# Performance work log

Measured on AMD Instinct MI355X. Metric: run time of the kernel, lower is better.

The kernel has to match this reference:

```python
import jax, jax.numpy as jnp
import numpy as np

EPS = 1e-5

def _mlp(x, W1, b1, W2, b2):
    h = jax.nn.gelu(x @ W1 + b1, approximate=False)
    return h @ W2 + b2

def _ln(x, g, b):
    m = jnp.mean(x, axis=-1, keepdims=True)
    v = jnp.mean((x - m) ** 2, axis=-1, keepdims=True)
    return (x - m) * jax.lax.rsqrt(v + EPS) * g + b

def setup_inputs() -> dict:
    key = jax.random.key(0)
    B, N, D = 4, 256, 128
    ks = jax.random.split(key, 32)
    s = 0.02
    inp = {
        "node_h": jax.random.normal(ks[0], (B, N, D), jnp.float32),
        "pair_h": jax.random.normal(ks[1], (B, N, N, D), jnp.float32),
        "node_mask": jax.random.randint(ks[2], (B, N), 0, 2, jnp.int32),
        "edge_mask": jax.random.randint(ks[3], (B, N, N), 0, 2, jnp.int32),
        # node_from_pair MLP: 3D -> 2D -> D
        "nfp_W1": jax.random.normal(ks[4], (3 * D, 2 * D), jnp.float32) * s,
        "nfp_b1": jnp.zeros((2 * D,), jnp.float32),
        "nfp_W2": jax.random.normal(ks[5], (2 * D, D), jnp.float32) * s,
        "nfp_b2": jnp.zeros((D,), jnp.float32),
        # pair_from_node MLP: 5D -> 2D -> D
        "pfn_W1": jax.random.normal(ks[6], (5 * D, 2 * D), jnp.float32) * s,
        "pfn_b1": jnp.zeros((2 * D,), jnp.float32),
        "pfn_W2": jax.random.normal(ks[7], (2 * D, D), jnp.float32) * s,
        "pfn_b2": jnp.zeros((D,), jnp.float32),
        # node_ff: D -> 4D -> D
        "nff_W1": jax.random.normal(ks[8], (D, 4 * D), jnp.float32) * s,
        "nff_b1": jnp.zeros((4 * D,), jnp.float32),
        "nff_W2": jax.random.normal(ks[9], (4 * D, D), jnp.float32) * s,
        "nff_b2": jnp.zeros((D,), jnp.float32),
        # pair_ff: D -> 4D -> D
        "pff_W1": jax.random.normal(ks[10], (D, 4 * D), jnp.float32) * s,
        "pff_b1": jnp.zeros((4 * D,), jnp.float32),
        "pff_W2": jax.random.normal(ks[11], (4 * D, D), jnp.float32) * s,
        "pff_b2": jnp.zeros((D,), jnp.float32),
        # gates: 2D -> D, sigmoid
        "og_W": jax.random.normal(ks[12], (2 * D, D), jnp.float32) * s,
        "og_b": jnp.zeros((D,), jnp.float32),
        "ig_W": jax.random.normal(ks[13], (2 * D, D), jnp.float32) * s,
        "ig_b": jnp.zeros((D,), jnp.float32),
        # LayerNorms
        "nn1_g": jnp.ones((D,), jnp.float32), "nn1_b": jnp.zeros((D,), jnp.float32),
        "nn2_g": jnp.ones((D,), jnp.float32), "nn2_b": jnp.zeros((D,), jnp.float32),
        "pn1_g": jnp.ones((D,), jnp.float32), "pn1_b": jnp.zeros((D,), jnp.float32),
        "pn2_g": jnp.ones((D,), jnp.float32), "pn2_b": jnp.zeros((D,), jnp.float32),
    }
    return inp

def reference(node_h, pair_h, node_mask, edge_mask,
              nfp_W1, nfp_b1, nfp_W2, nfp_b2,
              pfn_W1, pfn_b1, pfn_W2, pfn_b2,
              nff_W1, nff_b1, nff_W2, nff_b2,
              pff_W1, pff_b1, pff_W2, pff_b2,
              og_W, og_b, ig_W, ig_b,
              nn1_g, nn1_b, nn2_g, nn2_b,
              pn1_g, pn1_b, pn2_g, pn2_b):
    vp = edge_mask.astype(jnp.float32)                       # [B,N,N]
    pair_m = pair_h * vp[..., None]                          # masked pairs
    out_deg = jnp.clip(vp.sum(axis=2), 1.0)[..., None]       # [B,N,1]
    in_deg = jnp.clip(vp.sum(axis=1), 1.0)[..., None]        # [B,N,1]
    out_ctx_raw = pair_m.sum(axis=2) / out_deg               # [B,N,D]
    in_ctx_raw = pair_m.sum(axis=1) / in_deg                 # [B,N,D]
    out_g = jax.nn.sigmoid(jnp.concatenate([node_h, out_ctx_raw], -1) @ og_W + og_b)
    in_g = jax.nn.sigmoid(jnp.concatenate([node_h, in_ctx_raw], -1) @ ig_W + ig_b)
    node_upd = _mlp(jnp.concatenate([node_h, out_g * out_ctx_raw, in_g * in_ctx_raw], -1),
                    nfp_W1, nfp_b1, nfp_W2, nfp_b2)
    node_h = _ln(node_h + node_upd, nn1_g, nn1_b)
    node_h = _ln(node_h + _mlp(node_h, nff_W1, nff_b1, nff_W2, nff_b2), nn2_g, nn2_b)
    node_h = node_h * node_mask.astype(jnp.float32)[..., None]

    B, N, D = node_h.shape
    hi = jnp.broadcast_to(node_h[:, :, None, :], (B, N, N, D))
    hj = jnp.broadcast_to(node_h[:, None, :, :], (B, N, N, D))
    feat = jnp.concatenate([pair_h, hi, hj, hi - hj, hi * hj], -1)  # [B,N,N,5D]
    pair_upd = _mlp(feat, pfn_W1, pfn_b1, pfn_W2, pfn_b2)
    pair_h = _ln(pair_h + pair_upd, pn1_g, pn1_b)
    pair_h = _ln(pair_h + _mlp(pair_h, pff_W1, pff_b1, pff_W2, pff_b2), pn2_g, pn2_b)
    pair_h = pair_h * vp[..., None]
    return (node_h, pair_h)
```

## Files before the change

### kernel.cpp

```cpp
#include <hip/hip_runtime.h>
#include <hip/hip_bf16.h>

#define DI __device__ __forceinline__

typedef float f32x4 __attribute__((ext_vector_type(4)));
typedef float f32x2 __attribute__((ext_vector_type(2)));
typedef short s16x8 __attribute__((ext_vector_type(8)));
typedef short s16x4 __attribute__((ext_vector_type(4)));
typedef unsigned u32x2 __attribute__((ext_vector_type(2)));
typedef unsigned u32x4 __attribute__((ext_vector_type(4)));

DI short f2bf(float x) {
  union { float f; unsigned u; } v; v.f = x;
  unsigned r = v.u + 0x7fffu + ((v.u >> 16) & 1u);
  return (short)(r >> 16);
}

DI float bf2f(short x) {
  union { unsigned u; float f; } v;
  v.u = ((unsigned)(unsigned short)x) << 16;
  return v.f;
}

DI unsigned cvt_pk(float lo, float hi) {
  unsigned r;
  asm("v_cvt_pk_bf16_f32 %0, %1, %2" : "=v"(r) : "v"(lo), "v"(hi));
  return r;
}

DI s16x8 pack8(f32x4 a, f32x4 b) {
  union { u32x4 u; s16x8 s; } r;
  r.u[0] = cvt_pk(a[0], a[1]); r.u[1] = cvt_pk(a[2], a[3]);
  r.u[2] = cvt_pk(b[0], b[1]); r.u[3] = cvt_pk(b[2], b[3]);
  return r.s;
}

DI float gelu_f(float x) {
  const float e = __expf(-x * fmaf(x * x, 0.0713548162f, 1.5957691216f));
  return __fdividef(x, 1.f + e);
}

__global__ __launch_bounds__(256) void prep_ctx_kernel(
    const float* __restrict__ pair_h, const int* __restrict__ edge_mask,
    const float* __restrict__ pfnW1, const float* __restrict__ pfnW2,
    const float* __restrict__ pffW1, const float* __restrict__ pffW2,
    short* __restrict__ W1b, float* __restrict__ Wu, short* __restrict__ W2T,
    short* __restrict__ W1Tp, short* __restrict__ W2Tp,
    float* __restrict__ out_ctx, float* __restrict__ in_ctx) {
  __shared__ float sacc[2][128];
  __shared__ float sdeg[2];
  const int t = threadIdx.x;
  if (blockIdx.x >= 2048) {
    int idx = (blockIdx.x - 2048) * 256 + t;
    if (idx < 98304) {
      int n = idx / 384, k = idx % 384;
      float v;
      if (k < 128) v = pfnW1[k * 256 + n];
      else if (k < 256) v = pfnW1[(128 + k) * 256 + n] - pfnW1[(256 + k) * 256 + n];
      else v = pfnW1[(256 + k) * 256 + n];
      W1b[idx] = f2bf(v);
      return;
    }
    idx -= 98304;
    if (idx < 32768) {
      int k = idx / 256, n = idx % 256;
      Wu[idx] = pfnW1[(128 + k) * 256 + n] + pfnW1[(384 + k) * 256 + n];
      return;
    }
    idx -= 32768;
    if (idx < 32768) {
      int n = idx / 256, k = idx % 256;
      W2T[idx] = f2bf(pfnW2[k * 128 + n]);
      return;
    }
    idx -= 32768;
    if (idx < 65536) {
      int n = idx / 128, k = idx % 128;
      W1Tp[idx] = f2bf(pffW1[k * 512 + n]);
      return;
    }
    idx -= 65536;
    if (idx < 65536) {
      int n = idx / 512, k = idx % 512;
      W2Tp[idx] = f2bf(pffW2[k * 128 + n]);
    }
    return;
  }
  const int wg = blockIdx.x;
  const int half = t >> 7, d = t & 127;
  const bool outmode = wg < 1024;
  const int w2 = outmode ? wg : wg - 1024;
  const int b = w2 >> 8, x = w2 & 255;
  float acc = 0.f, deg = 0.f;
  for (int y0 = 0; y0 < 256; y0 += 2) {
    const int y = y0 + half;
    int row;
    if (outmode) row = (b * 256 + x) * 256 + y;
    else row = (b * 256 + y) * 256 + x;
    const int m = edge_mask[row];
    if (m) {
      acc += pair_h[(long)row * 128 + d];
      deg += 1.f;
    }
  }
  sacc[half][d] = acc;
  if (d == 0) sdeg[half] = deg;
  __syncthreads();
  if (t < 128) {
    float tot = sacc[0][d] + sacc[1][d];
    float dg = fmaxf(sdeg[0] + sdeg[1], 1.f);
    float* dst = outmode ? out_ctx : in_ctx;
    dst[(b * 256 + x) * 128 + d] = tot / dg;
  }
}

__global__ __launch_bounds__(256) void node_kernel(
    const float* __restrict__ node_h, const float* __restrict__ out_ctx,
    const float* __restrict__ in_ctx, const int* __restrict__ node_mask,
    const float* __restrict__ ogW, const float* __restrict__ ogb,
    const float* __restrict__ igW, const float* __restrict__ igb,
    const float* __restrict__ nW1, const float* __restrict__ nb1,
    const float* __restrict__ nW2, const float* __restrict__ nb2,
    const float* __restrict__ fW1, const float* __restrict__ fb1,
    const float* __restrict__ fW2, const float* __restrict__ fb2,
    const float* __restrict__ g1, const float* __restrict__ be1,
    const float* __restrict__ g2, const float* __restrict__ be2,
    const float* __restrict__ Wu, const float* __restrict__ ub1,
    float* __restrict__ out_node, short* __restrict__ node_bf,
    float* __restrict__ u_all) {
  __shared__ float sh[4][1792];
  __shared__ float fin[8][128];
  const int t = threadIdx.x;
  const int wv = t >> 6, lane = t & 63;
  float* const xn = sh[wv];
  float* const xo = sh[wv] + 256;
  float* const xi = sh[wv] + 512;
  float* const hh = sh[wv] + 768;
  const int row0 = blockIdx.x * 8 + wv * 2;

#pragma unroll
  for (int r = 0; r < 2; ++r) {
    const int row = row0 + r;
#pragma unroll
    for (int c = 0; c < 2; ++c) {
      const int col = lane + 64 * c;
      xn[r * 128 + col] = node_h[row * 128 + col];
      xo[r * 128 + col] = out_ctx[row * 128 + col];
      xi[r * 128 + col] = in_ctx[row * 128 + col];
    }
  }
  __syncthreads();

  {
    float ao[2][2], ai[2][2];
#pragma unroll
    for (int c = 0; c < 2; ++c) {
      const int col = lane + 64 * c;
      ao[0][c] = ao[1][c] = ogb[col];
      ai[0][c] = ai[1][c] = igb[col];
    }
    for (int k = 0; k < 256; ++k) {
      float xo0, xo1, xi0, xi1;
      if (k < 128) {
        xo0 = xi0 = xn[k];
        xo1 = xi1 = xn[128 + k];
      } else {
        xo0 = xo[k - 128]; xo1 = xo[k];
        xi0 = xi[k - 128]; xi1 = xi[k];
      }
#pragma unroll
      for (int c = 0; c < 2; ++c) {
        const int col = lane + 64 * c;
        const float wo = ogW[k * 128 + col], wi = igW[k * 128 + col];
        ao[0][c] += xo0 * wo; ao[1][c] += xo1 * wo;
        ai[0][c] += xi0 * wi; ai[1][c] += xi1 * wi;
      }
    }
#pragma unroll
    for (int c = 0; c < 2; ++c) {
      const int col = lane + 64 * c;
#pragma unroll
      for (int r = 0; r < 2; ++r) {
// ... 84 lines not shown
      }
    }
#pragma unroll
    for (int c = 0; c < 8; ++c) {
      const int col = lane + 64 * c;
      hh[col] = gelu_f(af[0][c]);
      hh[512 + col] = gelu_f(af[1][c]);
    }
  }
  __syncthreads();
  {
    float a2[2][2];
#pragma unroll
    for (int c = 0; c < 2; ++c) {
      const int col = lane + 64 * c;
      a2[0][c] = a2[1][c] = fb2[col];
    }
    for (int k = 0; k < 512; ++k) {
      const float h0 = hh[k], h1 = hh[512 + k];
#pragma unroll
      for (int c = 0; c < 2; ++c) {
        const int col = lane + 64 * c;
        const float w = fW2[k * 128 + col];
        a2[0][c] += h0 * w; a2[1][c] += h1 * w;
      }
    }
#pragma unroll
    for (int r = 0; r < 2; ++r) {
      const int row = row0 + r;
      float v0 = xn[r * 128 + lane] + a2[r][0];
      float v1 = xn[r * 128 + lane + 64] + a2[r][1];
      float s = v0 + v1, ss = v0 * v0 + v1 * v1;
#pragma unroll
      for (int off = 1; off < 64; off <<= 1) {
        s += __shfl_xor(s, off, 64);
        ss += __shfl_xor(ss, off, 64);
      }
      const float m = s * (1.f / 128.f);
      const float var = ss * (1.f / 128.f) - m * m;
      const float rs = rsqrtf(var + 1e-5f);
      const float msk = (float)node_mask[row];
      const float o0 = ((v0 - m) * rs * g2[lane] + be2[lane]) * msk;
      const float o1 = ((v1 - m) * rs * g2[lane + 64] + be2[lane + 64]) * msk;
      out_node[row * 128 + lane] = o0;
      out_node[row * 128 + lane + 64] = o1;
      node_bf[row * 128 + lane] = f2bf(o0);
      node_bf[row * 128 + lane + 64] = f2bf(o1);
      fin[wv * 2 + r][lane] = o0;
      fin[wv * 2 + r][lane + 64] = o1;
    }
  }
  __syncthreads();
  {
    float uacc[8];
    const float bb = ub1[t];
#pragma unroll
    for (int r = 0; r < 8; ++r) uacc[r] = bb;
#pragma unroll 4
    for (int k = 0; k < 128; ++k) {
      const float w = Wu[k * 256 + t];
#pragma unroll
      for (int r = 0; r < 8; ++r) uacc[r] += fin[r][k] * w;
    }
#pragma unroll
    for (int r = 0; r < 8; ++r)
      u_all[(blockIdx.x * 8 + r) * 256 + t] = uacc[r];
  }
}

__global__ __launch_bounds__(512, 4) void pair_kernel(
    const float* __restrict__ pair_h, const short* __restrict__ node_bf,
    const int* __restrict__ edge_mask, const short* __restrict__ W1b,
    const short* __restrict__ W2T, const short* __restrict__ W1Tp,
    const short* __restrict__ W2Tp, const float* __restrict__ u_all,
    const float* __restrict__ b2, const float* __restrict__ b1p,
    const float* __restrict__ b2p, const float* __restrict__ g1,
    const float* __restrict__ be1, const float* __restrict__ g2,
    const float* __restrict__ be2, float* __restrict__ out_pair) {
  constexpr int OFF_A = 0, OFF_H1 = 0, OFF_Y = 0, OFF_H2 = 16384,
                OFF_SCR = 49152;
  __shared__ __align__(16) char smem[51200];

  const int t = threadIdx.x;
  const int wg = blockIdx.x;
  const int b = wg >> 10, rem = wg & 1023;
  const int i = rem >> 2, j0 = (rem & 3) << 6;
  const int bi = (b << 8) + i;
  const long rowbase = (long)bi * 256 + j0;

  const int lane = t & 63, wv = t >> 6;
  const int lr = lane & 15, lq = lane >> 4;
  const int swz = (lr & 7) << 4;
  const int jb = (wv >> 2) * 32, nb2 = (wv & 3) * 32;

  {
    const int r = t >> 3, oc = t & 7, c0 = oc * 16;
    const int rsw = (r & 7) << 4;
    const float* prow = pair_h + (rowbase + r) * 128 + c0;
    const short* hjrow = node_bf + (b * 256 + j0 + r) * 128 + c0;
    const short* hirow = node_bf + (b * 256 + i) * 128 + c0;
    char* arow = smem + OFF_A + r * 768;
#pragma unroll
    for (int h = 0; h < 2; ++h) {
      f32x4 p0 = *(const f32x4*)(prow + h * 8);
      f32x4 p1 = *(const f32x4*)(prow + h * 8 + 4);
      s16x8 hj = *(const s16x8*)(hjrow + h * 8);
      s16x8 hi = *(const s16x8*)(hirow + h * 8);
      *(s16x8*)(arow + ((c0 * 2 + h * 16) ^ rsw)) = pack8(p0, p1);
      *(s16x8*)(arow + ((256 + c0 * 2 + h * 16) ^ rsw)) = hj;
      union { u32x4 u; s16x8 s; } pd;
#pragma unroll
      for (int e = 0; e < 4; ++e)
        pd.u[e] = cvt_pk(bf2f(hi[2 * e]) * bf2f(hj[2 * e]),
                         bf2f(hi[2 * e + 1]) * bf2f(hj[2 * e + 1]));
      *(s16x8*)(arow + ((512 + c0 * 2 + h * 16) ^ rsw)) = pd.s;
    }
  }
  __syncthreads();

  f32x4 acc1[4][2];
#pragma unroll
  for (int jt = 0; jt < 4; ++jt)
#pragma unroll
    for (int nt = 0; nt < 2; ++nt) acc1[jt][nt] = {0.f, 0.f, 0.f, 0.f};
  {
    const int nb = wv * 32;
    const short* wp0 = W1b + (nb + lr) * 384 + lq * 8;
    const short* wp1 = W1b + (nb + 16 + lr) * 384 + lq * 8;
    s16x8 w0p[4], w1p[4];
#pragma unroll
    for (int pf = 0; pf < 4; ++pf) {
      w0p[pf] = *(const s16x8*)(wp0 + pf * 32);
      w1p[pf] = *(const s16x8*)(wp1 + pf * 32);
    }
    s16x8 dc[4];
#pragma unroll
    for (int jt = 0; jt < 4; ++jt)
      dc[jt] = *(const s16x8*)(smem + OFF_A +
                               (((jt * 16 + lr) * 768 + lq * 16) ^ swz));
#pragma unroll
    for (int ks = 0; ks < 12; ++ks) {
      s16x8 w0 = w0p[ks & 3], w1 = w1p[ks & 3];
      if (ks < 8) {
        w0p[ks & 3] = *(const s16x8*)(wp0 + (ks + 4) * 32);
        w1p[ks & 3] = *(const s16x8*)(wp1 + (ks + 4) * 32);
      }
      s16x8 d[4];
#pragma unroll
      for (int jt = 0; jt < 4; ++jt) d[jt] = dc[jt];
      if (ks < 11) {
#pragma unroll
        for (int jt = 0; jt < 4; ++jt)
          dc[jt] = *(const s16x8*)(smem + OFF_A +
                                   (((jt * 16 + lr) * 768 + (ks + 1) * 64 + lq * 16) ^ swz));
      }
#pragma unroll
      for (int jt = 0; jt < 4; ++jt) {
        acc1[jt][0] = __builtin_amdgcn_mfma_f32_16x16x32_bf16(w0, d[jt], acc1[jt][0], 0, 0, 0);
        acc1[jt][1] = __builtin_amdgcn_mfma_f32_16x16x32_bf16(w1, d[jt], acc1[jt][1], 0, 0, 0);
      }
    }
  }
  f32x4 bu0 = *(const f32x4*)(u_all + bi * 256 + wv * 32 + lq * 4);
  f32x4 bu1 = *(const f32x4*)(u_all + bi * 256 + wv * 32 + 16 + lq * 4);
  const short* q2p0 = W2T + (nb2 + lr) * 256 + lq * 8;
  const short* q2p1 = W2T + (nb2 + 16 + lr) * 256 + lq * 8;
  s16x8 q2w0[4], q2w1[4];
  q2w0[0] = *(const s16x8*)q2p0;
  q2w1[0] = *(const s16x8*)q2p1;
  q2w0[1] = *(const s16x8*)(q2p0 + 32);
  q2w1[1] = *(const s16x8*)(q2p1 + 32);
  __syncthreads();
  {
    const int nb = wv * 32;
#pragma unroll
    for (int nt = 0; nt < 2; ++nt) {
      const int n0 = nb + nt * 16 + lq * 4;
      const f32x4 bu = nt ? bu1 : bu0;
#pragma unroll
      for (int jt = 0; jt < 4; ++jt) {
        const int j = jt * 16 + lr;
        u32x2 pk = {cvt_pk(gelu_f(acc1[jt][nt][0] + bu[0]),
                           gelu_f(acc1[jt][nt][1] + bu[1])),
                    cvt_pk(gelu_f(acc1[jt][nt][2] + bu[2]),
                           gelu_f(acc1[jt][nt][3] + bu[3]))};
        *(u32x2*)(smem + OFF_H1 + ((j * 512 + n0 * 2) ^ swz)) = pk;
      }
    }
  }
  __syncthreads();

  f32x4 x1v[2][2];
  {
    q2w0[2] = *(const s16x8*)(q2p0 + 64);
    q2w1[2] = *(const s16x8*)(q2p1 + 64);
    q2w0[3] = *(const s16x8*)(q2p0 + 96);
    q2w1[3] = *(const s16x8*)(q2p1 + 96);
    f32x4 pr[2][2];
#pragma unroll
    for (int nt = 0; nt < 2; ++nt)
#pragma unroll
      for (int jt = 0; jt < 2; ++jt)
        pr[jt][nt] = *(const f32x4*)(pair_h + (rowbase + jb + jt * 16 + lr) * 128 +
                                     nb2 + nt * 16 + lq * 4);
    s16x8 dc[2];
#pragma unroll
    for (int jt = 0; jt < 2; ++jt)
      dc[jt] = *(const s16x8*)(smem + OFF_H1 +
                               (((jb + jt * 16 + lr) * 512 + lq * 16) ^ swz));
    f32x4 acc2[2][2];
#pragma unroll
    for (int jt = 0; jt < 2; ++jt)
#pragma unroll
      for (int nt = 0; nt < 2; ++nt) acc2[jt][nt] = {0.f, 0.f, 0.f, 0.f};
#pragma unroll
    for (int ks = 0; ks < 8; ++ks) {
      s16x8 w0 = q2w0[ks & 3], w1 = q2w1[ks & 3];
      if (ks < 4) {
        q2w0[ks & 3] = *(const s16x8*)(q2p0 + (ks + 4) * 32);
        q2w1[ks & 3] = *(const s16x8*)(q2p1 + (ks + 4) * 32);
      }
      s16x8 d[2];
#pragma unroll
      for (int jt = 0; jt < 2; ++jt) d[jt] = dc[jt];
      if (ks < 7) {
#pragma unroll
        for (int jt = 0; jt < 2; ++jt)
          dc[jt] = *(const s16x8*)(smem + OFF_H1 +
                                   (((jb + jt * 16 + lr) * 512 + (ks + 1) * 64 + lq * 16) ^ swz));
      }
#pragma unroll
      for (int jt = 0; jt < 2; ++jt) {
        acc2[jt][0] = __builtin_amdgcn_mfma_f32_16x16x32_bf16(w0, d[jt], acc2[jt][0], 0, 0, 0);
        acc2[jt][1] = __builtin_amdgcn_mfma_f32_16x16x32_bf16(w1, d[jt], acc2[jt][1], 0, 0, 0);
      }
    }
#pragma unroll
    for (int nt = 0; nt < 2; ++nt) {
      const int n0 = nb2 + nt * 16 + lq * 4;
      f32x4 bv = *(const f32x4*)(b2 + n0);
#pragma unroll
      for (int jt = 0; jt < 2; ++jt)
        x1v[jt][nt] = acc2[jt][nt] + bv + pr[jt][nt];
    }
  }
  {
    float s[2], ss[2];
#pragma unroll
    for (int jt = 0; jt < 2; ++jt) {
      s[jt] = 0.f; ss[jt] = 0.f;
#pragma unroll
      for (int nt = 0; nt < 2; ++nt)
#pragma unroll
        for (int v = 0; v < 4; ++v) {
          const float x = x1v[jt][nt][v];
          s[jt] += x; ss[jt] += x * x;
        }
      s[jt] += __shfl_xor(s[jt], 16, 64);
      ss[jt] += __shfl_xor(ss[jt], 16, 64);
      s[jt] += __shfl_xor(s[jt], 32, 64);
      ss[jt] += __shfl_xor(ss[jt], 32, 64);
    }
    if (lq == 0) {
#pragma unroll
      for (int jt = 0; jt < 2; ++jt) {
        const int j = jb + jt * 16 + lr;
        f32x2 p = {s[jt], ss[jt]};
        *(f32x2*)(smem + OFF_SCR + j * 32 + (wv & 3) * 8) = p;
      }
    }
    __syncthreads();
    float lnm[2], lnr[2];
#pragma unroll
    for (int jt = 0; jt < 2; ++jt) {
      const int j = jb + jt * 16 + lr;
      f32x4 pA = *(const f32x4*)(smem + OFF_SCR + j * 32);
      f32x4 pB = *(const f32x4*)(smem + OFF_SCR + j * 32 + 16);
      const float S = pA[0] + pA[2] + pB[0] + pB[2];
      const float SS = pA[1] + pA[3] + pB[1] + pB[3];
      const float m = S * (1.f / 128.f);
      const float var = SS * (1.f / 128.f) - m * m;
      lnm[jt] = m;
      lnr[jt] = rsqrtf(var + 1e-5f);
    }
#pragma unroll
    for (int nt = 0; nt < 2; ++nt) {
      const int n0 = nb2 + nt * 16 + lq * 4;
      f32x4 gv = *(const f32x4*)(g1 + n0);
      f32x4 bv = *(const f32x4*)(be1 + n0);
#pragma unroll
      for (int jt = 0; jt < 2; ++jt) {
        const int j = jb + jt * 16 + lr;
        float y[4];
#pragma unroll
        for (int v = 0; v < 4; ++v)
          y[v] = (x1v[jt][nt][v] - lnm[jt]) * lnr[jt] * gv[v] + bv[v];
        u32x2 pk = {cvt_pk(y[0], y[1]), cvt_pk(y[2], y[3])};
        *(u32x2*)(smem + OFF_Y + ((j * 256 + n0 * 2) ^ swz)) = pk;
      }
    }
  }
  const short* g3p0a = W1Tp + (wv * 32 + lr) * 128 + lq * 8;
  const short* g3p1a = W1Tp + (wv * 32 + 16 + lr) * 128 + lq * 8;
  s16x8 g3w0[4], g3w1[4];
  g3w0[0] = *(const s16x8*)g3p0a;
  g3w1[0] = *(const s16x8*)g3p1a;
  g3w0[1] = *(const s16x8*)(g3p0a + 32);
  g3w1[1] = *(const s16x8*)(g3p1a + 32);
  const int em0 = edge_mask[rowbase + jb + lr];
  const int em1 = edge_mask[rowbase + jb + 16 + lr];
  __syncthreads();

  f32x4 acc4[2][2];
#pragma unroll
  for (int jt = 0; jt < 2; ++jt)
#pragma unroll
    for (int nt = 0; nt < 2; ++nt) acc4[jt][nt] = {0.f, 0.f, 0.f, 0.f};

#pragma unroll
  for (int p = 0; p < 2; ++p) {
    f32x4 acc3[4][2];
#pragma unroll
    for (int jt = 0; jt < 4; ++jt)
#pragma unroll
      for (int nt = 0; nt < 2; ++nt) acc3[jt][nt] = {0.f, 0.f, 0.f, 0.f};
    {
      const int nb3 = p * 256 + wv * 32;
      const short* wp0 = W1Tp + (nb3 + lr) * 128 + lq * 8;
      const short* wp1 = W1Tp + (nb3 + 16 + lr) * 128 + lq * 8;
      if (p == 0) {
        g3w0[2] = *(const s16x8*)(wp0 + 64);
        g3w1[2] = *(const s16x8*)(wp1 + 64);
        g3w0[3] = *(const s16x8*)(wp0 + 96);
        g3w1[3] = *(const s16x8*)(wp1 + 96);
      } else {
#pragma unroll
        for (int pf = 0; pf < 4; ++pf) {
          g3w0[pf] = *(const s16x8*)(wp0 + pf * 32);
          g3w1[pf] = *(const s16x8*)(wp1 + pf * 32);
        }
      }
#pragma unroll
      for (int ks = 0; ks < 4; ++ks) {
        s16x8 d[4];
#pragma unroll
        for (int jt = 0; jt < 4; ++jt)
          d[jt] = *(const s16x8*)(smem + OFF_Y +
                                  (((jt * 16 + lr) * 256 + ks * 64 + lq * 16) ^ swz));
#pragma unroll
        for (int jt = 0; jt < 4; ++jt) {
          acc3[jt][0] = __builtin_amdgcn_mfma_f32_16x16x32_bf16(g3w0[ks], d[jt], acc3[jt][0], 0, 0, 0);
          acc3[jt][1] = __builtin_amdgcn_mfma_f32_16x16x32_bf16(g3w1[ks], d[jt], acc3[jt][1], 0, 0, 0);
        }
      }
    }
    const short* qp0 = W2Tp + (nb2 + lr) * 512 + p * 256 + lq * 8;
    const short* qp1 = W2Tp + (nb2 + 16 + lr) * 512 + p * 256 + lq * 8;
    s16x8 q4w0[4], q4w1[4];
    q4w0[0] = *(const s16x8*)qp0;
    q4w1[0] = *(const s16x8*)qp1;
    q4w0[1] = *(const s16x8*)(qp0 + 32);
    q4w1[1] = *(const s16x8*)(qp1 + 32);
    if (p == 1) __syncthreads();
    {
#pragma unroll
      for (int nt = 0; nt < 2; ++nt) {
        const int n0l = wv * 32 + nt * 16 + lq * 4;
        f32x4 bv = *(const f32x4*)(b1p + p * 256 + n0l);
#pragma unroll
        for (int jt = 0; jt < 4; ++jt) {
          const int j = jt * 16 + lr;
          u32x2 pk = {cvt_pk(gelu_f(acc3[jt][nt][0] + bv[0]),
                             gelu_f(acc3[jt][nt][1] + bv[1])),
                      cvt_pk(gelu_f(acc3[jt][nt][2] + bv[2]),
                             gelu_f(acc3[jt][nt][3] + bv[3]))};
          *(u32x2*)(smem + OFF_H2 + ((j * 512 + n0l * 2) ^ swz)) = pk;
        }
      }
    }
    __syncthreads();
    {
      q4w0[2] = *(const s16x8*)(qp0 + 64);
      q4w1[2] = *(const s16x8*)(qp1 + 64);
      q4w0[3] = *(const s16x8*)(qp0 + 96);
      q4w1[3] = *(const s16x8*)(qp1 + 96);
      s16x8 dc[2];
#pragma unroll
      for (int jt = 0; jt < 2; ++jt)
        dc[jt] = *(const s16x8*)(smem + OFF_H2 +
                                 (((jb + jt * 16 + lr) * 512 + lq * 16) ^ swz));
#pragma unroll
      for (int ks = 0; ks < 8; ++ks) {
        s16x8 w0 = q4w0[ks & 3], w1 = q4w1[ks & 3];
        if (ks < 4) {
          q4w0[ks & 3] = *(const s16x8*)(qp0 + (ks + 4) * 32);
          q4w1[ks & 3] = *(const s16x8*)(qp1 + (ks + 4) * 32);
        }
        s16x8 d[2];
#pragma unroll
        for (int jt = 0; jt < 2; ++jt) d[jt] = dc[jt];
        if (ks < 7) {
#pragma unroll
          for (int jt = 0; jt < 2; ++jt)
            dc[jt] = *(const s16x8*)(smem + OFF_H2 +
                                     (((jb + jt * 16 + lr) * 512 + (ks + 1) * 64 + lq * 16) ^ swz));
        }
#pragma unroll
        for (int jt = 0; jt < 2; ++jt) {
          acc4[jt][0] = __builtin_amdgcn_mfma_f32_16x16x32_bf16(w0, d[jt], acc4[jt][0], 0, 0, 0);
          acc4[jt][1] = __builtin_amdgcn_mfma_f32_16x16x32_bf16(w1, d[jt], acc4[jt][1], 0, 0, 0);
        }
      }
    }
  }

  f32x4 x2v[2][2];
#pragma unroll
  for (int nt = 0; nt < 2; ++nt) {
    const int n0 = nb2 + nt * 16 + lq * 4;
    f32x4 bv = *(const f32x4*)(b2p + n0);
#pragma unroll
    for (int jt = 0; jt < 2; ++jt) {
      const int j = jb + jt * 16 + lr;
      s16x4 yv = *(const s16x4*)(smem + OFF_Y + ((j * 256 + n0 * 2) ^ swz));
      f32x4 yr;
#pragma unroll
      for (int v = 0; v < 4; ++v) yr[v] = bf2f(yv[v]);
      x2v[jt][nt] = acc4[jt][nt] + bv + yr;
    }
  }
  {
    float s[2], ss[2];
#pragma unroll
    for (int jt = 0; jt < 2; ++jt) {
      s[jt] = 0.f; ss[jt] = 0.f;
#pragma unroll
      for (int nt = 0; nt < 2; ++nt)
#pragma unroll
        for (int v = 0; v < 4; ++v) {
          const float x = x2v[jt][nt][v];
          s[jt] += x; ss[jt] += x * x;
        }
      s[jt] += __shfl_xor(s[jt], 16, 64);
      ss[jt] += __shfl_xor(ss[jt], 16, 64);
      s[jt] += __shfl_xor(s[jt], 32, 64);
      ss[jt] += __shfl_xor(ss[jt], 32, 64);
    }
    if (lq == 0) {
#pragma unroll
      for (int jt = 0; jt < 2; ++jt) {
        const int j = jb + jt * 16 + lr;
        f32x2 p = {s[jt], ss[jt]};
        *(f32x2*)(smem + OFF_SCR + j * 32 + (wv & 3) * 8) = p;
      }
    }
    __syncthreads();
    float lnm[2], lnr[2], vp[2];
#pragma unroll
    for (int jt = 0; jt < 2; ++jt) {
      const int j = jb + jt * 16 + lr;
      f32x4 pA = *(const f32x4*)(smem + OFF_SCR + j * 32);
      f32x4 pB = *(const f32x4*)(smem + OFF_SCR + j * 32 + 16);
      const float S = pA[0] + pA[2] + pB[0] + pB[2];
      const float SS = pA[1] + pA[3] + pB[1] + pB[3];
      const float m = S * (1.f / 128.f);
      const float var = SS * (1.f / 128.f) - m * m;
      lnm[jt] = m;
      lnr[jt] = rsqrtf(var + 1e-5f);
      vp[jt] = (float)(jt ? em1 : em0);
    }
#pragma unroll
    for (int nt = 0; nt < 2; ++nt) {
      const int n0 = nb2 + nt * 16 + lq * 4;
      f32x4 gv = *(const f32x4*)(g2 + n0);
      f32x4 bv = *(const f32x4*)(be2 + n0);
#pragma unroll
      for (int jt = 0; jt < 2; ++jt) {
        const int j = jb + jt * 16 + lr;
        f32x4 o;
#pragma unroll
        for (int v = 0; v < 4; ++v)
          o[v] = ((x2v[jt][nt][v] - lnm[jt]) * lnr[jt] * gv[v] + bv[v]) * vp[jt];
        *(f32x4*)(out_pair + (rowbase + j) * 128 + n0) = o;
      }
    }
  }
}

extern "C" void kernel_launch(void* const* d_in, const int* in_sizes, int n_in,
                              void* d_out, int out_size, void* d_ws,
                              size_t ws_size, hipStream_t stream) {
  const float* node_h = (const float*)d_in[0];
  const float* pair_h = (const float*)d_in[1];
  const int* node_mask = (const int*)d_in[2];
  const int* edge_mask = (const int*)d_in[3];
  const float* nfp_W1 = (const float*)d_in[4];
  const float* nfp_b1 = (const float*)d_in[5];
  const float* nfp_W2 = (const float*)d_in[6];
  const float* nfp_b2 = (const float*)d_in[7];
  const float* pfn_W1 = (const float*)d_in[8];
  const float* pfn_b1 = (const float*)d_in[9];
  const float* pfn_W2 = (const float*)d_in[10];
  const float* pfn_b2 = (const float*)d_in[11];
  const float* nff_W1 = (const float*)d_in[12];
  const float* nff_b1 = (const float*)d_in[13];
  const float* nff_W2 = (const float*)d_in[14];
  const float* nff_b2 = (const float*)d_in[15];
  const float* pff_W1 = (const float*)d_in[16];
  const float* pff_b1 = (const float*)d_in[17];
  const float* pff_W2 = (const float*)d_in[18];
  const float* pff_b2 = (const float*)d_in[19];
  const float* og_W = (const float*)d_in[20];
  const float* og_b = (const float*)d_in[21];
  const float* ig_W = (const float*)d_in[22];
  const float* ig_b = (const float*)d_in[23];
  const float* nn1_g = (const float*)d_in[24];
  const float* nn1_b = (const float*)d_in[25];
  const float* nn2_g = (const float*)d_in[26];
  const float* nn2_b = (const float*)d_in[27];
  const float* pn1_g = (const float*)d_in[28];
  const float* pn1_b = (const float*)d_in[29];
  const float* pn2_g = (const float*)d_in[30];
  const float* pn2_b = (const float*)d_in[31];

  char* ws = (char*)d_ws;
  short* W1b = (short*)(ws);
  short* W2T = (short*)(ws + 196608);
  short* W1Tp = (short*)(ws + 262144);
  short* W2Tp = (short*)(ws + 393216);
  float* Wu = (float*)(ws + 524288);
  float* out_ctx = (float*)(ws + 655360);
  float* in_ctx = (float*)(ws + 1179648);
  short* node_bf = (short*)(ws + 1703936);
  float* u_all = (float*)(ws + 1966080);

  float* out_node = (float*)d_out;
  float* out_pair = (float*)d_out + 131072;

  prep_ctx_kernel<<<3200, 256, 0, stream>>>(
      pair_h, edge_mask, pfn_W1, pfn_W2, pff_W1, pff_W2, W1b, Wu, W2T, W1Tp,
      W2Tp, out_ctx, in_ctx);
  node_kernel<<<128, 256, 0, stream>>>(
      node_h, out_ctx, in_ctx, node_mask, og_W, og_b, ig_W, ig_b, nfp_W1,
      nfp_b1, nfp_W2, nfp_b2, nff_W1, nff_b1, nff_W2, nff_b2, nn1_g, nn1_b,
      nn2_g, nn2_b, Wu, pfn_b1, out_node, node_bf, u_all);
  pair_kernel<<<4096, 512, 0, stream>>>(
      pair_h, node_bf, edge_mask, W1b, W2T, W1Tp, W2Tp, u_all, pfn_b2, pff_b1,
      pff_b2, pn1_g, pn1_b, pn2_g, pn2_b, out_pair);
}
```

Before: 597.8 us.

## Shrink pair kernel LDS by splitting first GEMM K and FFN hidden chunks

The 384-wide A tile of the first pair GEMM is now staged in two phases: pair_h and hj (256 columns) first, then the hi*hj product (128 columns) written over the same buffer. The pair FFN hidden layer is processed in four 128-wide chunks instead of two 256-wide chunks, which halves the H2 buffer. Shared memory drops from about 51 KB to 34 KB, which lets more 512-thread blocks fit per CU. In exchange the kernel runs more __syncthreads barriers and loses some of the register prefetch of weights.

```diff
diff --git a/kernel.cpp b/kernel.cpp
--- a/kernel.cpp
+++ b/kernel.cpp
@@ -344,8 +344,8 @@
     const float* __restrict__ be1, const float* __restrict__ g2,
     const float* __restrict__ be2, float* __restrict__ out_pair) {
   constexpr int OFF_A = 0, OFF_H1 = 0, OFF_Y = 0, OFF_H2 = 16384,
-                OFF_SCR = 49152;
-  __shared__ __align__(16) char smem[51200];
+                OFF_SCR = 32768;
+  __shared__ __align__(16) char smem[34816];
 
   const int t = threadIdx.x;
   const int wg = blockIdx.x;
@@ -359,27 +359,20 @@
   const int swz = (lr & 7) << 4;
   const int jb = (wv >> 2) * 32, nb2 = (wv & 3) * 32;
 
-  {
-    const int r = t >> 3, oc = t & 7, c0 = oc * 16;
-    const int rsw = (r & 7) << 4;
-    const float* prow = pair_h + (rowbase + r) * 128 + c0;
-    const short* hjrow = node_bf + (b * 256 + j0 + r) * 128 + c0;
-    const short* hirow = node_bf + (b * 256 + i) * 128 + c0;
-    char* arow = smem + OFF_A + r * 768;
+  const int r0 = t >> 3, oc0 = t & 7, c00 = oc0 * 16;
+  const int rsw0 = (r0 & 7) << 4;
+
+  {
+    const float* prow = pair_h + (rowbase + r0) * 128 + c00;
+    const short* hjrow = node_bf + (b * 256 + j0 + r0) * 128 + c00;
+    char* arow = smem + OFF_A + r0 * 512;
 #pragma unroll
     for (int h = 0; h < 2; ++h) {
       f32x4 p0 = *(const f32x4*)(prow + h * 8);
       f32x4 p1 = *(const f32x4*)(prow + h * 8 + 4);
       s16x8 hj = *(const s16x8*)(hjrow + h * 8);
-      s16x8 hi = *(const s16x8*)(hirow + h * 8);
-      *(s16x8*)(arow + ((c0 * 2 + h * 16) ^ rsw)) = pack8(p0, p1);
-      *(s16x8*)(arow + ((256 + c0 * 2 + h * 16) ^ rsw)) = hj;
-      union { u32x4 u; s16x8 s; } pd;
-#pragma unroll
-      for (int e = 0; e < 4; ++e)
-        pd.u[e] = cvt_pk(bf2f(hi[2 * e]) * bf2f(hj[2 * e]),
-                         bf2f(hi[2 * e + 1]) * bf2f(hj[2 * e + 1]));
-      *(s16x8*)(arow + ((512 + c0 * 2 + h * 16) ^ rsw)) = pd.s;
+      *(s16x8*)(arow + ((c00 * 2 + h * 16) ^ rsw0)) = pack8(p0, p1);
+      *(s16x8*)(arow + ((256 + c00 * 2 + h * 16) ^ rsw0)) = hj;
     }
   }
   __syncthreads();
@@ -403,23 +396,63 @@
 #pragma unroll
     for (int jt = 0; jt < 4; ++jt)
       dc[jt] = *(const s16x8*)(smem + OFF_A +
-                               (((jt * 16 + lr) * 768 + lq * 16) ^ swz));
-#pragma unroll
-    for (int ks = 0; ks < 12; ++ks) {
+                               (((jt * 16 + lr) * 512 + lq * 16) ^ swz));
+#pragma unroll
+    for (int ks = 0; ks < 8; ++ks) {
       s16x8 w0 = w0p[ks & 3], w1 = w1p[ks & 3];
-      if (ks < 8) {
+      if (ks < 4) {
         w0p[ks & 3] = *(const s16x8*)(wp0 + (ks + 4) * 32);
         w1p[ks & 3] = *(const s16x8*)(wp1 + (ks + 4) * 32);
       }
       s16x8 d[4];
 #pragma unroll
       for (int jt = 0; jt < 4; ++jt) d[jt] = dc[jt];
-      if (ks < 11) {
+      if (ks < 7) {
 #pragma unroll
         for (int jt = 0; jt < 4; ++jt)
           dc[jt] = *(const s16x8*)(smem + OFF_A +
-                                   (((jt * 16 + lr) * 768 + (ks + 1) * 64 + lq * 16) ^ swz));
-      }
+                                   (((jt * 16 + lr) * 512 + (ks + 1) * 64 + lq * 16) ^ swz));
+      }
+#pragma unroll
+      for (int jt = 0; jt < 4; ++jt) {
+        acc1[jt][0] = __builtin_amdgcn_mfma_f32_16x16x32_bf16(w0, d[jt], acc1[jt][0], 0, 0, 0);
+        acc1[jt][1] = __builtin_amdgcn_mfma_f32_16x16x32_bf16(w1, d[jt], acc1[jt][1], 0, 0, 0);
+      }
+    }
+  }
+  __syncthreads();
+
+  {
+    const short* hjrow = node_bf + (b * 256 + j0 + r0) * 128 + c00;
+    const short* hirow = node_bf + (b * 256 + i) * 128 + c00;
+    char* arow = smem + OFF_A + r0 * 256;
+#pragma unroll
+    for (int h = 0; h < 2; ++h) {
+      s16x8 hj = *(const s16x8*)(hjrow + h * 8);
+      s16x8 hi = *(const s16x8*)(hirow + h * 8);
+      union { u32x4 u; s16x8 s; } pd;
+#pragma unroll
+      for (int e = 0; e < 4; ++e)
+        pd.u[e] = cvt_pk(bf2f(hi[2 * e]) * bf2f(hj[2 * e]),
+                         bf2f(hi[2 * e + 1]) * bf2f(hj[2 * e + 1]));
+      *(s16x8*)(arow + ((c00 * 2 + h * 16) ^ rsw0)) = pd.s;
+    }
+  }
+  __syncthreads();
+
+  {
+    const int nb = wv * 32;
+    const short* wp0 = W1b + (nb + lr) * 384 + 256 + lq * 8;
+    const short* wp1 = W1b + (nb + 16 + lr) * 384 + 256 + lq * 8;
+#pragma unroll
+    for (int ks = 0; ks < 4; ++ks) {
+      s16x8 w0 = *(const s16x8*)(wp0 + ks * 32);
+      s16x8 w1 = *(const s16x8*)(wp1 + ks * 32);
+      s16x8 d[4];
+#pragma unroll
+      for (int jt = 0; jt < 4; ++jt)
+        d[jt] = *(const s16x8*)(smem + OFF_A +
+                                (((jt * 16 + lr) * 256 + ks * 64 + lq * 16) ^ swz));
 #pragma unroll
       for (int jt = 0; jt < 4; ++jt) {
         acc1[jt][0] = __builtin_amdgcn_mfma_f32_16x16x32_bf16(w0, d[jt], acc1[jt][0], 0, 0, 0);
@@ -566,13 +599,6 @@
       }
     }
   }
-  const short* g3p0a = W1Tp + (wv * 32 + lr) * 128 + lq * 8;
-  const short* g3p1a = W1Tp + (wv * 32 + 16 + lr) * 128 + lq * 8;
-  s16x8 g3w0[4], g3w1[4];
-  g3w0[0] = *(const s16x8*)g3p0a;
-  g3w1[0] = *(const s16x8*)g3p1a;
-  g3w0[1] = *(const s16x8*)(g3p0a + 32);
-  g3w1[1] = *(const s16x8*)(g3p1a + 32);
   const int em0 = edge_mask[rowbase + jb + lr];
   const int em1 = edge_mask[rowbase + jb + 16 + lr];
   __syncthreads();
@@ -584,92 +610,68 @@
     for (int nt = 0; nt < 2; ++nt) acc4[jt][nt] = {0.f, 0.f, 0.f, 0.f};
 
 #pragma unroll
-  for (int p = 0; p < 2; ++p) {
-    f32x4 acc3[4][2];
-#pragma unroll
-    for (int jt = 0; jt < 4; ++jt)
-#pragma unroll
-      for (int nt = 0; nt < 2; ++nt) acc3[jt][nt] = {0.f, 0.f, 0.f, 0.f};
+  for (int q = 0; q < 4; ++q) {
+    f32x4 acc3[4];
+#pragma unroll
+    for (int jt = 0; jt < 4; ++jt) acc3[jt] = {0.f, 0.f, 0.f, 0.f};
     {
-      const int nb3 = p * 256 + wv * 32;
-      const short* wp0 = W1Tp + (nb3 + lr) * 128 + lq * 8;
-      const short* wp1 = W1Tp + (nb3 + 16 + lr) * 128 + lq * 8;
-      if (p == 0) {
-        g3w0[2] = *(const s16x8*)(wp0 + 64);
-        g3w1[2] = *(const s16x8*)(wp1 + 64);
-        g3w0[3] = *(const s16x8*)(wp0 + 96);
-        g3w1[3] = *(const s16x8*)(wp1 + 96);
-      } else {
-#pragma unroll
-        for (int pf = 0; pf < 4; ++pf) {
-          g3w0[pf] = *(const s16x8*)(wp0 + pf * 32);
-          g3w1[pf] = *(const s16x8*)(wp1 + pf * 32);
-        }
-      }
+      const short* wp = W1Tp + (q * 128 + wv * 16 + lr) * 128 + lq * 8;
 #pragma unroll
       for (int ks = 0; ks < 4; ++ks) {
+        s16x8 w = *(const s16x8*)(wp + ks * 32);
         s16x8 d[4];
 #pragma unroll
         for (int jt = 0; jt < 4; ++jt)
           d[jt] = *(const s16x8*)(smem + OFF_Y +
                                   (((jt * 16 + lr) * 256 + ks * 64 + lq * 16) ^ swz));
 #pragma unroll
-        for (int jt = 0; jt < 4; ++jt) {
-          acc3[jt][0] = __builtin_amdgcn_mfma_f32_16x16x32_bf16(g3w0[ks], d[jt], acc3[jt][0], 0, 0, 0);
-          acc3[jt][1] = __builtin_amdgcn_mfma_f32_16x16x32_bf16(g3w1[ks], d[jt], acc3[jt][1], 0, 0, 0);
-        }
-      }
-    }
-    const short* qp0 = W2Tp + (nb2 + lr) * 512 + p * 256 + lq * 8;
-    const short* qp1 = W2Tp + (nb2 + 16 + lr) * 512 + p * 256 + lq * 8;
-    s16x8 q4w0[4], q4w1[4];
+        for (int jt = 0; jt < 4; ++jt)
+          acc3[jt] = __builtin_amdgcn_mfma_f32_16x16x32_bf16(w, d[jt], acc3[jt], 0, 0, 0);
+      }
+    }
+    const short* qp0 = W2Tp + (nb2 + lr) * 512 + q * 128 + lq * 8;
+    const short* qp1 = W2Tp + (nb2 + 16 + lr) * 512 + q * 128 + lq * 8;
+    s16x8 q4w0[2], q4w1[2];
     q4w0[0] = *(const s16x8*)qp0;
     q4w1[0] = *(const s16x8*)qp1;
     q4w0[1] = *(const s16x8*)(qp0 + 32);
     q4w1[1] = *(const s16x8*)(qp1 + 32);
-    if (p == 1) __syncthreads();
+    if (q > 0) __syncthreads();
     {
-#pragma unroll
-      for (int nt = 0; nt < 2; ++nt) {
-        const int n0l = wv * 32 + nt * 16 + lq * 4;
-        f32x4 bv = *(const f32x4*)(b1p + p * 256 + n0l);
-#pragma unroll
-        for (int jt = 0; jt < 4; ++jt) {
-          const int j = jt * 16 + lr;
-          u32x2 pk = {cvt_pk(gelu_f(acc3[jt][nt][0] + bv[0]),
-                             gelu_f(acc3[jt][nt][1] + bv[1])),
-                      cvt_pk(gelu_f(acc3[jt][nt][2] + bv[2]),
-                             gelu_f(acc3[jt][nt][3] + bv[3]))};
-          *(u32x2*)(smem + OFF_H2 + ((j * 512 + n0l * 2) ^ swz)) = pk;
-        }
+      const int l0 = wv * 16 + lq * 4;
+      f32x4 bv = *(const f32x4*)(b1p + q * 128 + l0);
+#pragma unroll
+      for (int jt = 0; jt < 4; ++jt) {
+        const int j = jt * 16 + lr;
+        u32x2 pk = {cvt_pk(gelu_f(acc3[jt][0] + bv[0]),
+                           gelu_f(acc3[jt][1] + bv[1])),
+                    cvt_pk(gelu_f(acc3[jt][2] + bv[2]),
+                           gelu_f(acc3[jt][3] + bv[3]))};
+        *(u32x2*)(smem + OFF_H2 + ((j * 256 + l0 * 2) ^ swz)) = pk;
       }
     }
     __syncthreads();
     {
-      q4w0[2] = *(const s16x8*)(qp0 + 64);
-      q4w1[2] = *(const s16x8*)(qp1 + 64);
-      q4w0[3] = *(const s16x8*)(qp0 + 96);
-      q4w1[3] = *(const s16x8*)(qp1 + 96);
       s16x8 dc[2];
 #pragma unroll
       for (int jt = 0; jt < 2; ++jt)
         dc[jt] = *(const s16x8*)(smem + OFF_H2 +
-                                 (((jb + jt * 16 + lr) * 512 + lq * 16) ^ swz));
-#pragma unroll
-      for (int ks = 0; ks < 8; ++ks) {
-        s16x8 w0 = q4w0[ks & 3], w1 = q4w1[ks & 3];
-        if (ks < 4) {
-          q4w0[ks & 3] = *(const s16x8*)(qp0 + (ks + 4) * 32);
-          q4w1[ks & 3] = *(const s16x8*)(qp1 + (ks + 4) * 32);
+                                 (((jb + jt * 16 + lr) * 256 + lq * 16) ^ swz));
+#pragma unroll
+      for (int ks = 0; ks < 4; ++ks) {
+        s16x8 w0 = q4w0[ks & 1], w1 = q4w1[ks & 1];
+        if (ks < 2) {
+          q4w0[ks & 1] = *(const s16x8*)(qp0 + (ks + 2) * 32);
+          q4w1[ks & 1] = *(const s16x8*)(qp1 + (ks + 2) * 32);
         }
         s16x8 d[2];
 #pragma unroll
         for (int jt = 0; jt < 2; ++jt) d[jt] = dc[jt];
-        if (ks < 7) {
+        if (ks < 3) {
 #pragma unroll
           for (int jt = 0; jt < 2; ++jt)
             dc[jt] = *(const s16x8*)(smem + OFF_H2 +
-                                     (((jb + jt * 16 + lr) * 512 + (ks + 1) * 64 + lq * 16) ^ swz));
+                                     (((jb + jt * 16 + lr) * 256 + (ks + 1) * 64 + lq * 16) ^ swz));
         }
 #pragma unroll
         for (int jt = 0; jt < 2; ++jt) {
```

New measurement: 601.2 us. No clear change (+0.6%).

## Precompute per-node hj projection to shrink first pair GEMM K from 384 to 256

Applied to the files above, without the earlier changes.

The hj-dependent part of the first pair MLP layer (hj·(W_hj − W_diff)) is now computed once per node in node_kernel and stored as bf16, so the per-pair GEMM only covers pair_h and hi*hj (K=256 instead of 384). The u vector is also stored as bf16, and the pair kernel reads the hjv row from global memory in its GELU epilogue. XOR-swizzled LDS addressing is replaced by padded row strides, which enlarges shared memory to about 68 KB and may reduce occupancy. The bf16 rounding of the precomputed terms adds a small precision risk.

```diff
diff --git a/kernel.cpp b/kernel.cpp
--- a/kernel.cpp
+++ b/kernel.cpp
@@ -44,27 +44,31 @@
     const float* __restrict__ pair_h, const int* __restrict__ edge_mask,
     const float* __restrict__ pfnW1, const float* __restrict__ pfnW2,
     const float* __restrict__ pffW1, const float* __restrict__ pffW2,
-    short* __restrict__ W1b, float* __restrict__ Wu, short* __restrict__ W2T,
-    short* __restrict__ W1Tp, short* __restrict__ W2Tp,
-    float* __restrict__ out_ctx, float* __restrict__ in_ctx) {
+    short* __restrict__ W1c, float* __restrict__ Wu, float* __restrict__ Whjv,
+    short* __restrict__ W2T, short* __restrict__ W1Tp,
+    short* __restrict__ W2Tp, float* __restrict__ out_ctx,
+    float* __restrict__ in_ctx) {
   __shared__ float sacc[2][128];
   __shared__ float sdeg[2];
   const int t = threadIdx.x;
   if (blockIdx.x >= 2048) {
     int idx = (blockIdx.x - 2048) * 256 + t;
-    if (idx < 98304) {
-      int n = idx / 384, k = idx % 384;
-      float v;
-      if (k < 128) v = pfnW1[k * 256 + n];
-      else if (k < 256) v = pfnW1[(128 + k) * 256 + n] - pfnW1[(256 + k) * 256 + n];
-      else v = pfnW1[(256 + k) * 256 + n];
-      W1b[idx] = f2bf(v);
+    if (idx < 65536) {
+      int n = idx / 256, k = idx % 256;
+      float v = (k < 128) ? pfnW1[k * 256 + n] : pfnW1[(384 + k) * 256 + n];
+      W1c[idx] = f2bf(v);
       return;
     }
-    idx -= 98304;
+    idx -= 65536;
     if (idx < 32768) {
       int k = idx / 256, n = idx % 256;
       Wu[idx] = pfnW1[(128 + k) * 256 + n] + pfnW1[(384 + k) * 256 + n];
+      return;
+    }
+    idx -= 32768;
+    if (idx < 32768) {
+      int k = idx / 256, n = idx % 256;
+      Whjv[idx] = pfnW1[(256 + k) * 256 + n] - pfnW1[(384 + k) * 256 + n];
       return;
     }
     idx -= 32768;
@@ -126,8 +130,9 @@
     const float* __restrict__ g1, const float* __restrict__ be1,
     const float* __restrict__ g2, const float* __restrict__ be2,
     const float* __restrict__ Wu, const float* __restrict__ ub1,
-    float* __restrict__ out_node, short* __restrict__ node_bf,
-    float* __restrict__ u_all) {
+    const float* __restrict__ Whjv, float* __restrict__ out_node,
+    short* __restrict__ node_bf, short* __restrict__ u_bf,
+    short* __restrict__ hjv_bf) {
   __shared__ float sh[4][1792];
   __shared__ float fin[8][128];
   const int t = threadIdx.x;
@@ -318,34 +323,42 @@
   }
   __syncthreads();
   {
-    float uacc[8];
+    float uacc[8], hacc[8];
     const float bb = ub1[t];
 #pragma unroll
-    for (int r = 0; r < 8; ++r) uacc[r] = bb;
+    for (int r = 0; r < 8; ++r) { uacc[r] = bb; hacc[r] = 0.f; }
 #pragma unroll 4
     for (int k = 0; k < 128; ++k) {
-      const float w = Wu[k * 256 + t];
-#pragma unroll
-      for (int r = 0; r < 8; ++r) uacc[r] += fin[r][k] * w;
-    }
-#pragma unroll
-    for (int r = 0; r < 8; ++r)
-      u_all[(blockIdx.x * 8 + r) * 256 + t] = uacc[r];
+      const float wu = Wu[k * 256 + t];
+      const float wh = Whjv[k * 256 + t];
+#pragma unroll
+      for (int r = 0; r < 8; ++r) {
+        uacc[r] += fin[r][k] * wu;
+        hacc[r] += fin[r][k] * wh;
+      }
+    }
+#pragma unroll
+    for (int r = 0; r < 8; ++r) {
+      u_bf[(blockIdx.x * 8 + r) * 256 + t] = f2bf(uacc[r]);
+      hjv_bf[(blockIdx.x * 8 + r) * 256 + t] = f2bf(hacc[r]);
+    }
   }
 }
 
 __global__ __launch_bounds__(512, 4) void pair_kernel(
     const float* __restrict__ pair_h, const short* __restrict__ node_bf,
-    const int* __restrict__ edge_mask, const short* __restrict__ W1b,
+    const int* __restrict__ edge_mask, const short* __restrict__ W1c,
     const short* __restrict__ W2T, const short* __restrict__ W1Tp,
-    const short* __restrict__ W2Tp, const float* __restrict__ u_all,
-    const float* __restrict__ b2, const float* __restrict__ b1p,
-    const float* __restrict__ b2p, const float* __restrict__ g1,
-    const float* __restrict__ be1, const float* __restrict__ g2,
-    const float* __restrict__ be2, float* __restrict__ out_pair) {
-  constexpr int OFF_A = 0, OFF_H1 = 0, OFF_Y = 0, OFF_H2 = 16384,
-                OFF_SCR = 49152;
-  __shared__ __align__(16) char smem[51200];
+    const short* __restrict__ W2Tp, const short* __restrict__ u_bf,
+    const short* __restrict__ hjv_bf, const float* __restrict__ b2,
+    const float* __restrict__ b1p, const float* __restrict__ b2p,
+    const float* __restrict__ g1, const float* __restrict__ be1,
+    const float* __restrict__ g2, const float* __restrict__ be2,
+    float* __restrict__ out_pair) {
+  constexpr int OFF_A = 0, OFF_H1 = 0, OFF_Y = 0, OFF_H2 = 33792,
+                OFF_SCR = 67584;
+  constexpr int PA = 528, PY = 272;
+  __shared__ __align__(16) char smem[69632];
 
   const int t = threadIdx.x;
   const int wg = blockIdx.x;
@@ -356,30 +369,27 @@
 
   const int lane = t & 63, wv = t >> 6;
   const int lr = lane & 15, lq = lane >> 4;
-  const int swz = (lr & 7) << 4;
   const int jb = (wv >> 2) * 32, nb2 = (wv & 3) * 32;
 
   {
     const int r = t >> 3, oc = t & 7, c0 = oc * 16;
-    const int rsw = (r & 7) << 4;
     const float* prow = pair_h + (rowbase + r) * 128 + c0;
     const short* hjrow = node_bf + (b * 256 + j0 + r) * 128 + c0;
     const short* hirow = node_bf + (b * 256 + i) * 128 + c0;
-    char* arow = smem + OFF_A + r * 768;
+    char* arow = smem + OFF_A + r * PA;
 #pragma unroll
     for (int h = 0; h < 2; ++h) {
       f32x4 p0 = *(const f32x4*)(prow + h * 8);
       f32x4 p1 = *(const f32x4*)(prow + h * 8 + 4);
       s16x8 hj = *(const s16x8*)(hjrow + h * 8);
       s16x8 hi = *(const s16x8*)(hirow + h * 8);
-      *(s16x8*)(arow + ((c0 * 2 + h * 16) ^ rsw)) = pack8(p0, p1);
-      *(s16x8*)(arow + ((256 + c0 * 2 + h * 16) ^ rsw)) = hj;
+      *(s16x8*)(arow + c0 * 2 + h * 16) = pack8(p0, p1);
       union { u32x4 u; s16x8 s; } pd;
 #pragma unroll
       for (int e = 0; e < 4; ++e)
         pd.u[e] = cvt_pk(bf2f(hi[2 * e]) * bf2f(hj[2 * e]),
                          bf2f(hi[2 * e + 1]) * bf2f(hj[2 * e + 1]));
-      *(s16x8*)(arow + ((512 + c0 * 2 + h * 16) ^ rsw)) = pd.s;
+      *(s16x8*)(arow + 256 + c0 * 2 + h * 16) = pd.s;
     }
   }
   __syncthreads();
@@ -391,8 +401,8 @@
     for (int nt = 0; nt < 2; ++nt) acc1[jt][nt] = {0.f, 0.f, 0.f, 0.f};
   {
     const int nb = wv * 32;
-    const short* wp0 = W1b + (nb + lr) * 384 + lq * 8;
-    const short* wp1 = W1b + (nb + 16 + lr) * 384 + lq * 8;
+    const short* wp0 = W1c + (nb + lr) * 256 + lq * 8;
+    const short* wp1 = W1c + (nb + 16 + lr) * 256 + lq * 8;
     s16x8 w0p[4], w1p[4];
 #pragma unroll
     for (int pf = 0; pf < 4; ++pf) {
@@ -402,23 +412,22 @@
     s16x8 dc[4];
 #pragma unroll
     for (int jt = 0; jt < 4; ++jt)
-      dc[jt] = *(const s16x8*)(smem + OFF_A +
-                               (((jt * 16 + lr) * 768 + lq * 16) ^ swz));
-#pragma unroll
-    for (int ks = 0; ks < 12; ++ks) {
+      dc[jt] = *(const s16x8*)(smem + OFF_A + (jt * 16 + lr) * PA + lq * 16);
+#pragma unroll
+    for (int ks = 0; ks < 8; ++ks) {
       s16x8 w0 = w0p[ks & 3], w1 = w1p[ks & 3];
-      if (ks < 8) {
+      if (ks < 4) {
         w0p[ks & 3] = *(const s16x8*)(wp0 + (ks + 4) * 32);
         w1p[ks & 3] = *(const s16x8*)(wp1 + (ks + 4) * 32);
       }
       s16x8 d[4];
 #pragma unroll
       for (int jt = 0; jt < 4; ++jt) d[jt] = dc[jt];
-      if (ks < 11) {
+      if (ks < 7) {
 #pragma unroll
         for (int jt = 0; jt < 4; ++jt)
-          dc[jt] = *(const s16x8*)(smem + OFF_A +
-                                   (((jt * 16 + lr) * 768 + (ks + 1) * 64 + lq * 16) ^ swz));
+          dc[jt] = *(const s16x8*)(smem + OFF_A + (jt * 16 + lr) * PA +
+                                   (ks + 1) * 64 + lq * 16);
       }
 #pragma unroll
       for (int jt = 0; jt < 4; ++jt) {
@@ -427,8 +436,8 @@
       }
     }
   }
-  f32x4 bu0 = *(const f32x4*)(u_all + bi * 256 + wv * 32 + lq * 4);
-  f32x4 bu1 = *(const f32x4*)(u_all + bi * 256 + wv * 32 + 16 + lq * 4);
+  s16x4 uv0 = *(const s16x4*)(u_bf + bi * 256 + wv * 32 + lq * 4);
+  s16x4 uv1 = *(const s16x4*)(u_bf + bi * 256 + wv * 32 + 16 + lq * 4);
   const short* q2p0 = W2T + (nb2 + lr) * 256 + lq * 8;
   const short* q2p1 = W2T + (nb2 + 16 + lr) * 256 + lq * 8;
   s16x8 q2w0[4], q2w1[4];
@@ -442,15 +451,21 @@
 #pragma unroll
     for (int nt = 0; nt < 2; ++nt) {
       const int n0 = nb + nt * 16 + lq * 4;
-      const f32x4 bu = nt ? bu1 : bu0;
+      const s16x4 uv = nt ? uv1 : uv0;
+      f32x4 uu;
+#pragma unroll
+      for (int v = 0; v < 4; ++v) uu[v] = bf2f(uv[v]);
 #pragma unroll
       for (int jt = 0; jt < 4; ++jt) {
         const int j = jt * 16 + lr;
-        u32x2 pk = {cvt_pk(gelu_f(acc1[jt][nt][0] + bu[0]),
-                           gelu_f(acc1[jt][nt][1] + bu[1])),
-                    cvt_pk(gelu_f(acc1[jt][nt][2] + bu[2]),
-                           gelu_f(acc1[jt][nt][3] + bu[3]))};
-        *(u32x2*)(smem + OFF_H1 + ((j * 512 + n0 * 2) ^ swz)) = pk;
+        s16x4 hv = *(const s16x4*)(hjv_bf + (b * 256 + j0 + j) * 256 + n0);
+        float pre[4];
+#pragma unroll
+        for (int v = 0; v < 4; ++v)
+          pre[v] = acc1[jt][nt][v] + uu[v] + bf2f(hv[v]);
+        u32x2 pk = {cvt_pk(gelu_f(pre[0]), gelu_f(pre[1])),
+                    cvt_pk(gelu_f(pre[2]), gelu_f(pre[3]))};
+        *(u32x2*)(smem + OFF_H1 + j * PA + n0 * 2) = pk;
       }
     }
   }
@@ -472,8 +487,7 @@
     s16x8 dc[2];
 #pragma unroll
     for (int jt = 0; jt < 2; ++jt)
-      dc[jt] = *(const s16x8*)(smem + OFF_H1 +
-                               (((jb + jt * 16 + lr) * 512 + lq * 16) ^ swz));
+      dc[jt] = *(const s16x8*)(smem + OFF_H1 + (jb + jt * 16 + lr) * PA + lq * 16);
     f32x4 acc2[2][2];
 #pragma unroll
     for (int jt = 0; jt < 2; ++jt)
@@ -492,8 +506,8 @@
       if (ks < 7) {
 #pragma unroll
         for (int jt = 0; jt < 2; ++jt)
-          dc[jt] = *(const s16x8*)(smem + OFF_H1 +
-                                   (((jb + jt * 16 + lr) * 512 + (ks + 1) * 64 + lq * 16) ^ swz));
+          dc[jt] = *(const s16x8*)(smem + OFF_H1 + (jb + jt * 16 + lr) * PA +
+                                   (ks + 1) * 64 + lq * 16);
       }
 #pragma unroll
       for (int jt = 0; jt < 2; ++jt) {
@@ -562,7 +576,7 @@
         for (int v = 0; v < 4; ++v)
           y[v] = (x1v[jt][nt][v] - lnm[jt]) * lnr[jt] * gv[v] + bv[v];
         u32x2 pk = {cvt_pk(y[0], y[1]), cvt_pk(y[2], y[3])};
-        *(u32x2*)(smem + OFF_Y + ((j * 256 + n0 * 2) ^ swz)) = pk;
+        *(u32x2*)(smem + OFF_Y + j * PY + n0 * 2) = pk;
       }
     }
   }
@@ -611,8 +625,8 @@
         s16x8 d[4];
 #pragma unroll
         for (int jt = 0; jt < 4; ++jt)
-          d[jt] = *(const s16x8*)(smem + OFF_Y +
-                                  (((jt * 16 + lr) * 256 + ks * 64 + lq * 16) ^ swz));
+          d[jt] = *(const s16x8*)(smem + OFF_Y + (jt * 16 + lr) * PY +
+                                  ks * 64 + lq * 16);
 #pragma unroll
         for (int jt = 0; jt < 4; ++jt) {
           acc3[jt][0] = __builtin_amdgcn_mfma_f32_16x16x32_bf16(g3w0[ks], d[jt], acc3[jt][0], 0, 0, 0);
@@ -640,7 +654,7 @@
                              gelu_f(acc3[jt][nt][1] + bv[1])),
                       cvt_pk(gelu_f(acc3[jt][nt][2] + bv[2]),
                              gelu_f(acc3[jt][nt][3] + bv[3]))};
-          *(u32x2*)(smem + OFF_H2 + ((j * 512 + n0l * 2) ^ swz)) = pk;
+          *(u32x2*)(smem + OFF_H2 + j * PA + n0l * 2) = pk;
         }
       }
     }
@@ -653,8 +667,7 @@
       s16x8 dc[2];
 #pragma unroll
       for (int jt = 0; jt < 2; ++jt)
-        dc[jt] = *(const s16x8*)(smem + OFF_H2 +
-                                 (((jb + jt * 16 + lr) * 512 + lq * 16) ^ swz));
+        dc[jt] = *(const s16x8*)(smem + OFF_H2 + (jb + jt * 16 + lr) * PA + lq * 16);
 #pragma unroll
       for (int ks = 0; ks < 8; ++ks) {
         s16x8 w0 = q4w0[ks & 3], w1 = q4w1[ks & 3];
@@ -668,8 +681,8 @@
         if (ks < 7) {
 #pragma unroll
           for (int jt = 0; jt < 2; ++jt)
-            dc[jt] = *(const s16x8*)(smem + OFF_H2 +
-                                     (((jb + jt * 16 + lr) * 512 + (ks + 1) * 64 + lq * 16) ^ swz));
+            dc[jt] = *(const s16x8*)(smem + OFF_H2 + (jb + jt * 16 + lr) * PA +
+                                     (ks + 1) * 64 + lq * 16);
         }
 #pragma unroll
         for (int jt = 0; jt < 2; ++jt) {
@@ -688,7 +701,7 @@
 #pragma unroll
     for (int jt = 0; jt < 2; ++jt) {
       const int j = jb + jt * 16 + lr;
-      s16x4 yv = *(const s16x4*)(smem + OFF_Y + ((j * 256 + n0 * 2) ^ swz));
+      s16x4 yv = *(const s16x4*)(smem + OFF_Y + j * PY + n0 * 2);
       f32x4 yr;
 #pragma unroll
       for (int v = 0; v < 4; ++v) yr[v] = bf2f(yv[v]);
@@ -790,27 +803,29 @@
   const float* pn2_b = (const float*)d_in[31];
 
   char* ws = (char*)d_ws;
-  short* W1b = (short*)(ws);
-  short* W2T = (short*)(ws + 196608);
-  short* W1Tp = (short*)(ws + 262144);
-  short* W2Tp = (short*)(ws + 393216);
-  float* Wu = (float*)(ws + 524288);
-  float* out_ctx = (float*)(ws + 655360);
-  float* in_ctx = (float*)(ws + 1179648);
-  short* node_bf = (short*)(ws + 1703936);
-  float* u_all = (float*)(ws + 1966080);
+  short* W1c = (short*)(ws);
+  short* W2T = (short*)(ws + 131072);
+  short* W1Tp = (short*)(ws + 196608);
+  short* W2Tp = (short*)(ws + 327680);
+  float* Wu = (float*)(ws + 458752);
+  float* Whjv = (float*)(ws + 589824);
+  float* out_ctx = (float*)(ws + 720896);
+  float* in_ctx = (float*)(ws + 1245184);
+  short* node_bf = (short*)(ws + 1769472);
+  short* u_bf = (short*)(ws + 2031616);
+  short* hjv_bf = (short*)(ws + 2555904);
 
   float* out_node = (float*)d_out;
   float* out_pair = (float*)d_out + 131072;
 
   prep_ctx_kernel<<<3200, 256, 0, stream>>>(
-      pair_h, edge_mask, pfn_W1, pfn_W2, pff_W1, pff_W2, W1b, Wu, W2T, W1Tp,
-      W2Tp, out_ctx, in_ctx);
+      pair_h, edge_mask, pfn_W1, pfn_W2, pff_W1, pff_W2, W1c, Wu, Whjv, W2T,
+      W1Tp, W2Tp, out_ctx, in_ctx);
   node_kernel<<<128, 256, 0, stream>>>(
       node_h, out_ctx, in_ctx, node_mask, og_W, og_b, ig_W, ig_b, nfp_W1,
       nfp_b1, nfp_W2, nfp_b2, nff_W1, nff_b1, nff_W2, nff_b2, nn1_g, nn1_b,
-      nn2_g, nn2_b, Wu, pfn_b1, out_node, node_bf, u_all);
+      nn2_g, nn2_b, Wu, pfn_b1, Whjv, out_node, node_bf, u_bf, hjv_bf);
   pair_kernel<<<4096, 512, 0, stream>>>(
-      pair_h, node_bf, edge_mask, W1b, W2T, W1Tp, W2Tp, u_all, pfn_b2, pff_b1,
-      pff_b2, pn1_g, pn1_b, pn2_g, pn2_b, out_pair);
+      pair_h, node_bf, edge_mask, W1c, W2T, W1Tp, W2Tp, u_bf, hjv_bf, pfn_b2,
+      pff_b1, pff_b2, pn1_g, pn1_b, pn2_g, pn2_b, out_pair);
 }
```

After: 602.1 us. About the same (+0.7%).
